# Kernel tuning notes

Measured on AMD Instinct MI355X. Metric: run time of the kernel, lower is better.

Reference implementation:

```python
import jax, jax.numpy as jnp
import numpy as np

D = 1024      # hidden_dim
H = 16        # num_heads
KV = 8        # num_kv_heads
HD = D // H   # head_size = 64
M = 3584      # intermediate_dim
E = 8         # num_local_experts
TOPK = 2      # num_experts_per_tok
EPS = 1e-6
ROPE_THETA = 10000.0


def setup_inputs() -> dict:
    key = jax.random.key(0)
    ks = jax.random.split(key, 12)
    s = 0.02
    B, S = 2, 1024
    return {
        "x": jax.random.normal(ks[0], (B, S, D), jnp.float32),
        "ln1_w": jnp.ones((D,), jnp.float32),
        "ln2_w": jnp.ones((D,), jnp.float32),
        "wq": jax.random.normal(ks[1], (D, H * HD), jnp.float32) * s,
        "wk": jax.random.normal(ks[2], (D, KV * HD), jnp.float32) * s,
        "wv": jax.random.normal(ks[3], (D, KV * HD), jnp.float32) * s,
        "wo": jax.random.normal(ks[4], (H * HD, D), jnp.float32) * s,
        "router_w": jax.random.normal(ks[5], (D, E), jnp.float32) * s,
        "w_gate": jax.random.normal(ks[6], (E, D, M), jnp.float32) * s,
        "w_up": jax.random.normal(ks[7], (E, D, M), jnp.float32) * s,
        "w_down": jax.random.normal(ks[8], (E, M, D), jnp.float32) * s,
    }


def _rmsnorm(x, w, eps=EPS):
    xf = x.astype(jnp.float32)
    var = jnp.mean(xf * xf, axis=-1, keepdims=True)
    return (xf * jax.lax.rsqrt(var + eps)).astype(x.dtype) * w


def _rope(q, k):
    # q: [B,S,H,HD], k: [B,S,KV,HD]
    S = q.shape[1]
    inv_freq = 1.0 / (ROPE_THETA ** (jnp.arange(0, HD, 2, dtype=jnp.float32) / HD))
    ang = jnp.arange(S, dtype=jnp.float32)[:, None] * inv_freq[None, :]  # [S, HD/2]
    cos = jnp.concatenate([jnp.cos(ang), jnp.cos(ang)], axis=-1)[None, :, None, :]
    sin = jnp.concatenate([jnp.sin(ang), jnp.sin(ang)], axis=-1)[None, :, None, :]

    def rot_half(t):
        t1, t2 = jnp.split(t, 2, axis=-1)
        return jnp.concatenate([-t2, t1], axis=-1)

    return q * cos + rot_half(q) * sin, k * cos + rot_half(k) * sin


def reference(x, ln1_w, ln2_w, wq, wk, wv, wo, router_w, w_gate, w_up, w_down):
    B, S, _ = x.shape

    # ---- self-attention block ----
    h = _rmsnorm(x, ln1_w)
    q = (h @ wq).reshape(B, S, H, HD)
    k = (h @ wk).reshape(B, S, KV, HD)
    v = (h @ wv).reshape(B, S, KV, HD)
    q, k = _rope(q, k)
    rep = H // KV
    k = jnp.repeat(k, rep, axis=2)  # [B,S,H,HD]
    v = jnp.repeat(v, rep, axis=2)
    scores = jnp.einsum("bqhd,bkhd->bhqk", q, k) / jnp.sqrt(jnp.float32(HD))
    causal = jnp.tril(jnp.ones((S, S), bool))
    scores = jnp.where(causal[None, None], scores, jnp.finfo(scores.dtype).min)
    attn = jax.nn.softmax(scores, axis=-1)
    ao = jnp.einsum("bhqk,bkhd->bqhd", attn, v).reshape(B, S, H * HD)
    x = x + ao @ wo

    # ---- sparse MoE block (top-2 routing, SwiGLU experts) ----
    h = _rmsnorm(x, ln2_w)
    logits = h @ router_w                       # [B,S,E]
    probs = jax.nn.softmax(logits, axis=-1)
    topv, topi = jax.lax.top_k(probs, TOPK)     # [B,S,K]
    topv = topv / jnp.sum(topv, axis=-1, keepdims=True)
    # dense combine weights [B,S,E]: zero for unselected experts
    weights = jnp.sum(jax.nn.one_hot(topi, E, dtype=h.dtype) * topv[..., None], axis=-2)
    gate = jnp.einsum("bsd,edm->bsem", h, w_gate)
    up = jnp.einsum("bsd,edm->bsem", h, w_up)
    act = jax.nn.silu(gate) * up * weights[..., None]
    moe = jnp.einsum("bsem,emd->bsd", act, w_down)
    return x + moe
```

## Files before the change

kernel.cpp:

```cpp
#include <hip/hip_runtime.h>

typedef __attribute__((ext_vector_type(8))) short short8;
typedef __attribute__((ext_vector_type(4))) float f32x4;
typedef unsigned int u32;

#define DI static __device__ __forceinline__

DI unsigned short f2bf(float f) {
  unsigned u = __builtin_bit_cast(unsigned, f);
  u += 0x7fffu + ((u >> 16) & 1u);
  return (unsigned short)(u >> 16);
}
DI float bf2f(unsigned short b) {
  unsigned u = ((unsigned)b) << 16;
  return __builtin_bit_cast(float, u);
}

DI void gload16(const unsigned short* g, unsigned short* l) {
  __builtin_amdgcn_global_load_lds(
      (const __attribute__((address_space(1))) u32*)g,
      (__attribute__((address_space(3))) u32*)l, 16, 0, 0);
}

static constexpr int NT   = 2048;
static constexpr int SEQ  = 1024;
static constexpr int DIM  = 1024;
static constexpr int NH   = 16;
static constexpr int NKV  = 8;
static constexpr int HD   = 64;
static constexpr int MDIM = 3584;
static constexpr int NE   = 8;
static constexpr int QW   = 2048;
static constexpr int GUW  = 2 * MDIM;

__global__ void __launch_bounds__(256) transpose_kernel(
    const float* __restrict__ in, unsigned short* __restrict__ out,
    int R, int C, size_t in_estride, size_t out_estride) {
  __shared__ unsigned short tl[64][66];
  int e = blockIdx.z;
  const float* ip = in + (size_t)e * in_estride;
  unsigned short* op = out + (size_t)e * out_estride;
  int c0 = blockIdx.x * 64, r0 = blockIdx.y * 64;
  int tid = threadIdx.x;
  {
    int lr = tid >> 4, lc = (tid & 15) * 4;
#pragma unroll
    for (int p = 0; p < 4; ++p) {
      int r = p * 16 + lr;
      float4 v = *(const float4*)(ip + (size_t)(r0 + r) * C + c0 + lc);
      tl[lc + 0][r] = f2bf(v.x);
      tl[lc + 1][r] = f2bf(v.y);
      tl[lc + 2][r] = f2bf(v.z);
      tl[lc + 3][r] = f2bf(v.w);
    }
  }
  __syncthreads();
  {
    int c = tid >> 2, rc = (tid & 3) * 16;
    unsigned short tmp[16];
#pragma unroll
    for (int j = 0; j < 8; ++j) {
      u32 w = *(const u32*)&tl[c][rc + j * 2];
      tmp[j * 2] = (unsigned short)w;
      tmp[j * 2 + 1] = (unsigned short)(w >> 16);
    }
    unsigned short* dst = op + (size_t)(c0 + c) * R + r0 + rc;
#pragma unroll
    for (int j = 0; j < 2; ++j)
      *(uint4*)(dst + j * 8) = *(const uint4*)&tmp[j * 8];
  }
}

__global__ void __launch_bounds__(256) rmsnorm_kernel(const float* __restrict__ x,
                                                      const float* __restrict__ w,
                                                      unsigned short* __restrict__ out) {
  int row = blockIdx.x;
  const float* xr = x + (size_t)row * DIM;
  int i = threadIdx.x * 4;
  float4 v = *(const float4*)(xr + i);
  float s = v.x * v.x + v.y * v.y + v.z * v.z + v.w * v.w;
  for (int o = 32; o; o >>= 1) s += __shfl_xor(s, o);
  __shared__ float red[4];
  if ((threadIdx.x & 63) == 0) red[threadIdx.x >> 6] = s;
  __syncthreads();
  s = red[0] + red[1] + red[2] + red[3];
  float r = rsqrtf(s * (1.0f / DIM) + 1e-6f);
  float4 wv = *(const float4*)(w + i);
  ushort4 o4;
  o4.x = f2bf(v.x * r * wv.x);
  o4.y = f2bf(v.y * r * wv.y);
  o4.z = f2bf(v.z * r * wv.z);
  o4.w = f2bf(v.w * r * wv.w);
  *(ushort4*)(out + (size_t)row * DIM + i) = o4;
}

template <int GATHER, int EPI>
__global__ void __launch_bounds__(256) gemmT_kernel(
    const unsigned short* __restrict__ A, int lda,
    const unsigned short* __restrict__ B, int ldb, size_t b_estride,
    void* __restrict__ Cv, int ldc,
    const float* __restrict__ resid,
    int M, int K,
    const int* __restrict__ lists, const int* __restrict__ cnt) {
  int e = blockIdx.z;
  int count = M;
  const int* lst = nullptr;
  if (GATHER != 0) {
    count = cnt[e];
    if (count <= 0) return;
    lst = lists + e * NT;
    B += b_estride * (size_t)e;
  }
  int m0 = blockIdx.y * 128;
  if (m0 >= count) return;
  int n0 = blockIdx.x * 128;

  __shared__ unsigned short sA[3][128 * 32];
  __shared__ unsigned short sB[3][128 * 32];

  int tid = threadIdx.x, w = tid >> 6, lane = tid & 63;
  int l15 = lane & 15, lhi = lane >> 4;

  int srow = w * 16 + (lane >> 2);
  int schunk = ((lane & 3) ^ ((lane >> 2) & 3)) * 8;
  const unsigned short *aSrc0, *aSrc1, *bSrc0, *bSrc1;
  {
    int mr0 = m0 + srow, mr1 = m0 + 64 + srow;
    int ar0, ar1;
    if (GATHER == 0) { ar0 = mr0; ar1 = mr1; }
    else {
      int c0i = mr0 < count ? mr0 : count - 1;
      int c1i = mr1 < count ? mr1 : count - 1;
      int p0 = lst[c0i], p1 = lst[c1i];
      ar0 = (GATHER == 1) ? (p0 >> 1) : p0;
      ar1 = (GATHER == 1) ? (p1 >> 1) : p1;
    }
    aSrc0 = A + (size_t)ar0 * lda + schunk;
    aSrc1 = A + (size_t)ar1 * lda + schunk;
    bSrc0 = B + (size_t)(n0 + srow) * ldb + schunk;
    bSrc1 = B + (size_t)(n0 + 64 + srow) * ldb + schunk;
  }
  unsigned ldst = (unsigned)(w * 16) * 32;

#define STAGE(buf, k0)                                   \
  do {                                                   \
    gload16(aSrc0 + (k0), &sA[buf][ldst]);               \
    gload16(aSrc1 + (k0), &sA[buf][ldst + 64 * 32]);     \
    gload16(bSrc0 + (k0), &sB[buf][ldst]);               \
    gload16(bSrc1 + (k0), &sB[buf][ldst + 64 * 32]);     \
  } while (0)

  f32x4 acc[4][4] = {};
  int wm = w >> 1, wn = w & 1;
  int aoff[4], boff[4];
#pragma unroll
  for (int t = 0; t < 4; ++t) {
    int row = wm * 64 + t * 16 + l15;
    aoff[t] = row * 32 + ((lhi ^ (row & 3)) * 8);
    int col = wn * 64 + t * 16 + l15;
    boff[t] = col * 32 + ((lhi ^ (col & 3)) * 8);
  }

  int nsteps = K / 32;
  STAGE(0, 0);
  if (nsteps > 1) STAGE(1, 32);

  int cur = 0, stg = 2;
  for (int t = 0; t < nsteps; ++t) {
    if (t + 1 < nsteps) asm volatile("s_waitcnt vmcnt(4)" ::: "memory");
    else                asm volatile("s_waitcnt vmcnt(0)" ::: "memory");
    __builtin_amdgcn_s_barrier();
    __builtin_amdgcn_sched_barrier(0);
    if (t + 2 < nsteps) STAGE(stg, (t + 2) * 32);
    const unsigned short* pa = sA[cur];
    const unsigned short* pb = sB[cur];
    short8 af[4], bfr[4];
#pragma unroll
    for (int q = 0; q < 4; ++q) {
      af[q] = *(const short8*)&pa[aoff[q]];
      bfr[q] = *(const short8*)&pb[boff[q]];
    }
    __builtin_amdgcn_s_setprio(1);
#pragma unroll
    for (int mi = 0; mi < 4; ++mi)
#pragma unroll
      for (int ni = 0; ni < 4; ++ni)
        acc[mi][ni] =
            __builtin_amdgcn_mfma_f32_16x16x32_bf16(af[mi], bfr[ni], acc[mi][ni], 0, 0, 0);
    __builtin_amdgcn_s_setprio(0);
    cur = (cur == 2) ? 0 : cur + 1;
    stg = (stg == 2) ? 0 : stg + 1;
  }
#undef STAGE

#pragma unroll
  for (int mi = 0; mi < 4; ++mi) {
#pragma unroll
    for (int r = 0; r < 4; ++r) {
      int mr = m0 + wm * 64 + mi * 16 + lhi * 4 + r;
      if (GATHER != 0 && mr >= count) continue;
      size_t crow = (GATHER != 0) ? (size_t)lst[mr] : (size_t)mr;
#pragma unroll
      for (int ni = 0; ni < 4; ++ni) {
        int n = n0 + wn * 64 + ni * 16 + l15;
        float val = acc[mi][ni][r];
        if (EPI == 0)
          ((unsigned short*)Cv)[crow * ldc + n] = f2bf(val);
        else if (EPI == 1)
          ((float*)Cv)[crow * ldc + n] = val + resid[crow * ldc + n];
        else
          ((float*)Cv)[crow * ldc + n] = val;
      }
    }
  }
}

__global__ void __launch_bounds__(256) rope_kernel(unsigned short* __restrict__ qkv) {
  int g = blockIdx.x * 256 + threadIdx.x;
  int i = g & 31;
  int hh = (g >> 5) % (NH + NKV);
  int tok = g / (32 * (NH + NKV));
  if (tok >= NT) return;
  int s = tok & (SEQ - 1);
  float inv = exp2f((float)i * (-13.287712379549449f / 32.0f));
  float ang = (float)s * inv;
  float sn = sinf(ang);
  float c = cosf(ang);
  int col = (hh < NH) ? hh * HD : DIM + (hh - NH) * HD;
  unsigned short* ptr = qkv + (size_t)tok * QW + col;
  float a = bf2f(ptr[i]), b2 = bf2f(ptr[i + 32]);
  ptr[i] = f2bf(a * c - b2 * sn);
  ptr[i + 32] = f2bf(b2 * c + a * sn);
}

__global__ void __launch_bounds__(64) attn_kernel(const unsigned short* __restrict__ qkv,
                                                  unsigned short* __restrict__ ao) {
  __shared__ unsigned short Ps[16 * 64];
  int bid = blockIdx.x;
  int qt = bid & 63;
  int h = (bid >> 6) & 15;
  int b = bid >> 10;
  int lane = threadIdx.x, l15 = lane & 15, lhi = lane >> 4;
  int q0 = qt * 16, kvh = h >> 1;
  int kcol = DIM + kvh * HD, vcol = DIM + NKV * HD + kvh * HD;

  const unsigned short* qp = qkv + ((size_t)(b * SEQ + q0 + l15)) * QW + h * HD + lhi * 8;
  short8 aq0 = *(const short8*)qp;
  short8 aq1 = *(const short8*)(qp + 32);

  float m[4] = {-1e30f, -1e30f, -1e30f, -1e30f};
  float l[4] = {0.f, 0.f, 0.f, 0.f};
  f32x4 accO[4] = {};

  int nkb = (qt >> 2) + 1;
  for (int kb_ = 0; kb_ < nkb; ++kb_) {
    int kbase = kb_ * 64;
    f32x4 s[4];
#pragma unroll
    for (int ct = 0; ct < 4; ++ct) {
      const unsigned short* kp =
          qkv + ((size_t)(b * SEQ + kbase + ct * 16 + l15)) * QW + kcol + lhi * 8;
      short8 k0v = *(const short8*)kp;
      short8 k1v = *(const short8*)(kp + 32);
      f32x4 a = {};
      a = __builtin_amdgcn_mfma_f32_16x16x32_bf16(aq0, k0v, a, 0, 0, 0);
      a = __builtin_amdgcn_mfma_f32_16x16x32_bf16(aq1, k1v, a, 0, 0, 0);
      int kpos = kbase + ct * 16 + l15;
#pragma unroll
      for (int r = 0; r < 4; ++r) {
        float v = a[r] * 0.125f;
        if (kpos > q0 + lhi * 4 + r) v = -1e30f;
        s[ct][r] = v;
      }
    }
    float nm[4], al[4], rs[4];
#pragma unroll
    for (int r = 0; r < 4; ++r) {
      float mb = fmaxf(fmaxf(s[0][r], s[1][r]), fmaxf(s[2][r], s[3][r]));
      mb = fmaxf(mb, __shfl_xor(mb, 1));
      mb = fmaxf(mb, __shfl_xor(mb, 2));
      mb = fmaxf(mb, __shfl_xor(mb, 4));
      mb = fmaxf(mb, __shfl_xor(mb, 8));
      nm[r] = fmaxf(m[r], mb);
      al[r] = __expf(m[r] - nm[r]);
      m[r] = nm[r];
      rs[r] = 0.f;
    }
#pragma unroll
    for (int ct = 0; ct < 4; ++ct) {
#pragma unroll
      for (int r = 0; r < 4; ++r) {
        float p = __expf(s[ct][r] - nm[r]);
        rs[r] += p;
        int q = lhi * 4 + r;
        Ps[q * 64 + ((ct * 16 + l15) ^ (lhi << 4))] = f2bf(p);
      }
    }
#pragma unroll
    for (int r = 0; r < 4; ++r) {
      rs[r] += __shfl_xor(rs[r], 1);
      rs[r] += __shfl_xor(rs[r], 2);
      rs[r] += __shfl_xor(rs[r], 4);
      rs[r] += __shfl_xor(rs[r], 8);
      l[r] = l[r] * al[r] + rs[r];
    }
#pragma unroll
    for (int dt = 0; dt < 4; ++dt)
#pragma unroll
      for (int r = 0; r < 4; ++r) accO[dt][r] *= al[r];

    int pswz = (l15 >> 2) << 4;
    short8 ap0 = *(const short8*)&Ps[l15 * 64 + ((lhi * 8) ^ pswz)];
    short8 ap1 = *(const short8*)&Ps[l15 * 64 + ((32 + lhi * 8) ^ pswz)];
#pragma unroll
    for (int dt = 0; dt < 4; ++dt) {
#pragma unroll
      for (int ks = 0; ks < 2; ++ks) {
        const unsigned short* vp =
            qkv + ((size_t)(b * SEQ + kbase + ks * 32 + lhi * 8)) * QW + vcol + dt * 16 + l15;
        short8 vf;
#pragma unroll
        for (int j = 0; j < 8; ++j) vf[j] = (short)vp[(size_t)j * QW];
        accO[dt] = __builtin_amdgcn_mfma_f32_16x16x32_bf16(ks ? ap1 : ap0, vf, accO[dt], 0, 0, 0);
      }
    }
  }
  float invl[4];
#pragma unroll
  for (int r = 0; r < 4; ++r) invl[r] = 1.f / l[r];
#pragma unroll
  for (int dt = 0; dt < 4; ++dt)
#pragma unroll
    for (int r = 0; r < 4; ++r)
      ao[((size_t)(b * SEQ + q0 + lhi * 4 + r)) * DIM + h * HD + dt * 16 + l15] =
          f2bf(accO[dt][r] * invl[r]);
}

__global__ void zero_cnt_kernel(int* __restrict__ cnt) {
  if (threadIdx.x < NE) cnt[threadIdx.x] = 0;
}

__global__ void __launch_bounds__(64) router_kernel(const float* __restrict__ x2,
                                                    const float* __restrict__ ln2w,
                                                    const float* __restrict__ rw,
                                                    float* __restrict__ wts,
                                                    int* __restrict__ cnt,
                                                    int* __restrict__ lists) {
  int t = blockIdx.x, lane = threadIdx.x;
  const float* xr = x2 + (size_t)t * DIM;
  float xs[16];
  double ssq = 0.0;
#pragma unroll
  for (int j = 0; j < 16; ++j) {
    xs[j] = xr[lane + j * 64];
    ssq += (double)xs[j] * xs[j];
  }
  for (int o = 32; o; o >>= 1) ssq += __shfl_xor(ssq, o);
  double r = rsqrt(ssq * (1.0 / DIM) + 1e-6);
  double p[NE] = {};
#pragma unroll
  for (int j = 0; j < 16; ++j) {
    int i = lane + j * 64;
    double hv = (double)xs[j] * r * (double)ln2w[i];
    const float* rwp = rw + (size_t)i * NE;
#pragma unroll
    for (int e = 0; e < NE; ++e) p[e] += hv * (double)rwp[e];
  }
  for (int o = 32; o; o >>= 1) {
#pragma unroll
    for (int e = 0; e < NE; ++e) p[e] += __shfl_xor(p[e], o);
  }
  if (lane == 0) {
    int i1 = 0;
    for (int e = 1; e < NE; ++e)
      if (p[e] > p[i1]) i1 = e;
    int i2 = (i1 == 0) ? 1 : 0;
    for (int e = 0; e < NE; ++e)
      if (e != i1 && p[e] > p[i2]) i2 = e;
    double mx = fmax(p[i1], p[i2]);
    double e1 = exp(p[i1] - mx), e2 = exp(p[i2] - mx);
    double inv = 1.0 / (e1 + e2);
    wts[t * 2] = (float)(e1 * inv);
    wts[t * 2 + 1] = (float)(e2 * inv);
    int pos1 = atomicAdd(&cnt[i1], 1);
    lists[i1 * NT + pos1] = t * 2;
    int pos2 = atomicAdd(&cnt[i2], 1);
    lists[i2 * NT + pos2] = t * 2 + 1;
  }
}

__global__ void __launch_bounds__(256) swiglu_kernel(const unsigned short* __restrict__ gu,
                                                     const float* __restrict__ wts,
                                                     unsigned short* __restrict__ act) {
  size_t i = ((size_t)blockIdx.x * 256 + threadIdx.x) * 8;
  int pid = (int)(i / MDIM);
  int mcol = (int)(i - (size_t)pid * MDIM);
  float w = wts[pid];
  const unsigned short* row = gu + (size_t)pid * GUW;
  short8 g8 = *(const short8*)(row + mcol);
  short8 u8 = *(const short8*)(row + MDIM + mcol);
  short8 o8;
#pragma unroll
  for (int j = 0; j < 8; ++j) {
    float gv = bf2f((unsigned short)g8[j]);
    float uv = bf2f((unsigned short)u8[j]);
    float sv = gv / (1.f + __expf(-gv));
    o8[j] = (short)f2bf(sv * uv * w);
  }
  *(short8*)(act + i) = o8;
}

__global__ void __launch_bounds__(256) combine_kernel(const float* __restrict__ x2,
                                                      const float* __restrict__ part,
                                                      float* __restrict__ out) {
  size_t idx = ((size_t)blockIdx.x * 256 + threadIdx.x) * 4;
  size_t t = idx >> 10;
  size_t d = idx & 1023;
  float4 a = *(const float4*)(x2 + idx);
  float4 b = *(const float4*)(part + (t * 2) * DIM + d);
  float4 c = *(const float4*)(part + (t * 2 + 1) * DIM + d);
  float4 o;
  o.x = a.x + b.x + c.x;
  o.y = a.y + b.y + c.y;
  o.z = a.z + b.z + c.z;
  o.w = a.w + b.w + c.w;
  *(float4*)(out + idx) = o;
}

extern "C" void kernel_launch(void* const* d_in, const int* in_sizes, int n_in,
                              void* d_out, int out_size, void* d_ws, size_t ws_size,
                              hipStream_t stream) {
  const float* x   = (const float*)d_in[0];
  const float* ln1 = (const float*)d_in[1];
  const float* ln2 = (const float*)d_in[2];
  const float* wq  = (const float*)d_in[3];
  const float* wk  = (const float*)d_in[4];
  const float* wv  = (const float*)d_in[5];
  const float* wo  = (const float*)d_in[6];
  const float* rw  = (const float*)d_in[7];
  const float* wg  = (const float*)d_in[8];
  const float* wu  = (const float*)d_in[9];
  const float* wd  = (const float*)d_in[10];
  float* out = (float*)d_out;

  char* p = (char*)d_ws;
  auto take = [&](size_t bytes) {
    char* q = p;
    p += (bytes + 255) & ~(size_t)255;
    return q;
  };
  unsigned short* wguT = (unsigned short*)take((size_t)NE * GUW * DIM * 2);
  unsigned short* wdT  = (unsigned short*)take((size_t)NE * DIM * MDIM * 2);
  float*          x2   = (float*)take((size_t)NT * DIM * 4);
  unsigned short* h2   = (unsigned short*)take((size_t)NT * DIM * 2);
  float*          part = (float*)take((size_t)2 * NT * DIM * 4);
  unsigned short* act  = (unsigned short*)take((size_t)2 * NT * MDIM * 2);
  float*          wtsb = (float*)take((size_t)2 * NT * 4);
  int*            cntb = (int*)take(NE * 4);
  int*            listsb = (int*)take((size_t)NE * NT * 4);
  char* X = p;
  unsigned short* wqkvT = (unsigned short*)X;
  unsigned short* woT   = wqkvT + (size_t)QW * DIM;
  unsigned short* h1    = woT + (size_t)DIM * DIM;
  unsigned short* qkv   = h1 + (size_t)NT * DIM;
  unsigned short* aob   = qkv + (size_t)NT * QW;
  unsigned short* gu    = (unsigned short*)X;

  transpose_kernel<<<dim3(16, 16, 1), 256, 0, stream>>>(wq, wqkvT, DIM, DIM, 0, 0);
  transpose_kernel<<<dim3(8, 16, 1), 256, 0, stream>>>(wk, wqkvT + (size_t)DIM * DIM, DIM, 512, 0, 0);
  transpose_kernel<<<dim3(8, 16, 1), 256, 0, stream>>>(wv, wqkvT + (size_t)(DIM + 512) * DIM, DIM, 512, 0, 0);
  transpose_kernel<<<dim3(16, 16, 1), 256, 0, stream>>>(wo, woT, DIM, DIM, 0, 0);
  transpose_kernel<<<dim3(56, 16, NE), 256, 0, stream>>>(
      wg, wguT, DIM, MDIM, (size_t)DIM * MDIM, (size_t)GUW * DIM);
  transpose_kernel<<<dim3(56, 16, NE), 256, 0, stream>>>(
      wu, wguT + (size_t)MDIM * DIM, DIM, MDIM, (size_t)DIM * MDIM, (size_t)GUW * DIM);
  transpose_kernel<<<dim3(16, 56, NE), 256, 0, stream>>>(
      wd, wdT, MDIM, DIM, (size_t)MDIM * DIM, (size_t)DIM * MDIM);

  rmsnorm_kernel<<<NT, 256, 0, stream>>>(x, ln1, h1);
  gemmT_kernel<0, 0><<<dim3(QW / 128, NT / 128, 1), 256, 0, stream>>>(
      h1, DIM, wqkvT, DIM, 0, qkv, QW, nullptr, NT, DIM, nullptr, nullptr);
  rope_kernel<<<(NT * (NH + NKV) * 32) / 256, 256, 0, stream>>>(qkv);
  attn_kernel<<<NT * NH / 16, 64, 0, stream>>>(qkv, aob);
  gemmT_kernel<0, 1><<<dim3(DIM / 128, NT / 128, 1), 256, 0, stream>>>(
      aob, DIM, woT, DIM, 0, x2, DIM, x, NT, DIM, nullptr, nullptr);

  rmsnorm_kernel<<<NT, 256, 0, stream>>>(x2, ln2, h2);
  zero_cnt_kernel<<<1, 64, 0, stream>>>(cntb);
  router_kernel<<<NT, 64, 0, stream>>>(x2, ln2, rw, wtsb, cntb, listsb);

  gemmT_kernel<1, 0><<<dim3(GUW / 128, 16, NE), 256, 0, stream>>>(
      h2, DIM, wguT, DIM, (size_t)GUW * DIM, gu, GUW, nullptr, 0, DIM, listsb, cntb);
  swiglu_kernel<<<(int)(((size_t)2 * NT * MDIM) / (256 * 8)), 256, 0, stream>>>(
      gu, wtsb, act);
  gemmT_kernel<2, 2><<<dim3(DIM / 128, 16, NE), 256, 0, stream>>>(
      act, MDIM, wdT, MDIM, (size_t)DIM * MDIM, part, DIM, nullptr, 0, MDIM, listsb, cntb);

  combine_kernel<<<(NT * DIM) / 1024, 256, 0, stream>>>(x2, part, out);
}
```

Before: 564.5 us.

## Widen gate/up GEMM tile to 256 columns and split-K the down projection

The GEMM kernel gets a compile-time N-tile width. The MoE gate/up projection now uses 128x256 tiles, which raises A-tile reuse and halves the number of gathered-row blocks, at the cost of more registers and LDS. The down projection is split along K into two halves across the z grid dimension, which doubles its block count for better CU occupancy. Each half writes to its own partial buffer and the combine kernel sums both halves, adding extra memory traffic and workspace.

```diff
diff --git a/kernel.cpp b/kernel.cpp
--- a/kernel.cpp
+++ b/kernel.cpp
@@ -94,15 +94,22 @@
   *(ushort4*)(out + (size_t)row * DIM + i) = o4;
 }
 
-template <int GATHER, int EPI>
+template <int GATHER, int EPI, int NNT>
 __global__ void __launch_bounds__(256) gemmT_kernel(
     const unsigned short* __restrict__ A, int lda,
     const unsigned short* __restrict__ B, int ldb, size_t b_estride,
     void* __restrict__ Cv, int ldc,
     const float* __restrict__ resid,
     int M, int K,
-    const int* __restrict__ lists, const int* __restrict__ cnt) {
-  int e = blockIdx.z;
+    const int* __restrict__ lists, const int* __restrict__ cnt,
+    int ks_count, size_t ks_stride) {
+  constexpr int BN = NNT * 32;
+  constexpr int NBLK = BN / 64;
+  int zz = blockIdx.z;
+  int e = zz / ks_count, ks = zz - e * ks_count;
+  int KL = K / ks_count;
+  int kbase = ks * KL;
+
   int count = M;
   const int* lst = nullptr;
   if (GATHER != 0) {
@@ -113,17 +120,18 @@
   }
   int m0 = blockIdx.y * 128;
   if (m0 >= count) return;
-  int n0 = blockIdx.x * 128;
+  int n0 = blockIdx.x * BN;
 
   __shared__ unsigned short sA[3][128 * 32];
-  __shared__ unsigned short sB[3][128 * 32];
+  __shared__ unsigned short sB[3][BN * 32];
 
   int tid = threadIdx.x, w = tid >> 6, lane = tid & 63;
   int l15 = lane & 15, lhi = lane >> 4;
 
   int srow = w * 16 + (lane >> 2);
   int schunk = ((lane & 3) ^ ((lane >> 2) & 3)) * 8;
-  const unsigned short *aSrc0, *aSrc1, *bSrc0, *bSrc1;
+  const unsigned short *aSrc0, *aSrc1;
+  const unsigned short* bSrc[NBLK];
   {
     int mr0 = m0 + srow, mr1 = m0 + 64 + srow;
     int ar0, ar1;
@@ -135,63 +143,69 @@
       ar0 = (GATHER == 1) ? (p0 >> 1) : p0;
       ar1 = (GATHER == 1) ? (p1 >> 1) : p1;
     }
-    aSrc0 = A + (size_t)ar0 * lda + schunk;
-    aSrc1 = A + (size_t)ar1 * lda + schunk;
-    bSrc0 = B + (size_t)(n0 + srow) * ldb + schunk;
-    bSrc1 = B + (size_t)(n0 + 64 + srow) * ldb + schunk;
+    aSrc0 = A + (size_t)ar0 * lda + kbase + schunk;
+    aSrc1 = A + (size_t)ar1 * lda + kbase + schunk;
+#pragma unroll
+    for (int s = 0; s < NBLK; ++s)
+      bSrc[s] = B + (size_t)(n0 + s * 64 + srow) * ldb + kbase + schunk;
   }
   unsigned ldst = (unsigned)(w * 16) * 32;
 
-#define STAGE(buf, k0)                                   \
-  do {                                                   \
-    gload16(aSrc0 + (k0), &sA[buf][ldst]);               \
-    gload16(aSrc1 + (k0), &sA[buf][ldst + 64 * 32]);     \
-    gload16(bSrc0 + (k0), &sB[buf][ldst]);               \
-    gload16(bSrc1 + (k0), &sB[buf][ldst + 64 * 32]);     \
-  } while (0)
-
-  f32x4 acc[4][4] = {};
+  auto stage = [&](int buf, int k0) {
+    gload16(aSrc0 + k0, &sA[buf][ldst]);
+    gload16(aSrc1 + k0, &sA[buf][ldst + 64 * 32]);
+#pragma unroll
+    for (int s = 0; s < NBLK; ++s)
+      gload16(bSrc[s] + k0, &sB[buf][ldst + s * 64 * 32]);
+  };
+
+  f32x4 acc[4][NNT] = {};
   int wm = w >> 1, wn = w & 1;
-  int aoff[4], boff[4];
+  int aoff[4], boff[NNT];
 #pragma unroll
   for (int t = 0; t < 4; ++t) {
     int row = wm * 64 + t * 16 + l15;
     aoff[t] = row * 32 + ((lhi ^ (row & 3)) * 8);
-    int col = wn * 64 + t * 16 + l15;
+  }
+#pragma unroll
+  for (int t = 0; t < NNT; ++t) {
+    int col = wn * (BN / 2) + t * 16 + l15;
     boff[t] = col * 32 + ((lhi ^ (col & 3)) * 8);
   }
 
-  int nsteps = K / 32;
-  STAGE(0, 0);
-  if (nsteps > 1) STAGE(1, 32);
+  int nsteps = KL / 32;
+  stage(0, 0);
+  if (nsteps > 1) stage(1, 32);
 
   int cur = 0, stg = 2;
   for (int t = 0; t < nsteps; ++t) {
-    if (t + 1 < nsteps) asm volatile("s_waitcnt vmcnt(4)" ::: "memory");
-    else                asm volatile("s_waitcnt vmcnt(0)" ::: "memory");
+    if (t + 1 < nsteps) {
+      if constexpr (NNT == 8) asm volatile("s_waitcnt vmcnt(6)" ::: "memory");
+      else                    asm volatile("s_waitcnt vmcnt(4)" ::: "memory");
+    } else {
+      asm volatile("s_waitcnt vmcnt(0)" ::: "memory");
+    }
     __builtin_amdgcn_s_barrier();
     __builtin_amdgcn_sched_barrier(0);
-    if (t + 2 < nsteps) STAGE(stg, (t + 2) * 32);
+    if (t + 2 < nsteps) stage(stg, (t + 2) * 32);
     const unsigned short* pa = sA[cur];
     const unsigned short* pb = sB[cur];
-    short8 af[4], bfr[4];
-#pragma unroll
-    for (int q = 0; q < 4; ++q) {
-      af[q] = *(const short8*)&pa[aoff[q]];
-      bfr[q] = *(const short8*)&pb[boff[q]];
-    }
+    short8 af[4], bfr[NNT];
+#pragma unroll
+    for (int q = 0; q < 4; ++q) af[q] = *(const short8*)&pa[aoff[q]];
+#pragma unroll
+    for (int q = 0; q < NNT; ++q) bfr[q] = *(const short8*)&pb[boff[q]];
     __builtin_amdgcn_s_setprio(1);
 #pragma unroll
     for (int mi = 0; mi < 4; ++mi)
 #pragma unroll
-      for (int ni = 0; ni < 4; ++ni)
+      for (int ni = 0; ni < NNT; ++ni)
         acc[mi][ni] =
             __builtin_amdgcn_mfma_f32_16x16x32_bf16(af[mi], bfr[ni], acc[mi][ni], 0, 0, 0);
     __builtin_amdgcn_s_setprio(0);
     cur = (cur == 2) ? 0 : cur + 1;
     stg = (stg == 2) ? 0 : stg + 1;
   }
-#undef STAGE
 
 #pragma unroll
   for (int mi = 0; mi < 4; ++mi) {
@@ -201,15 +215,15 @@
       if (GATHER != 0 && mr >= count) continue;
       size_t crow = (GATHER != 0) ? (size_t)lst[mr] : (size_t)mr;
 #pragma unroll
-      for (int ni = 0; ni < 4; ++ni) {
-        int n = n0 + wn * 64 + ni * 16 + l15;
+      for (int ni = 0; ni < NNT; ++ni) {
+        int n = n0 + wn * (BN / 2) + ni * 16 + l15;
         float val = acc[mi][ni][r];
         if (EPI == 0)
           ((unsigned short*)Cv)[crow * ldc + n] = f2bf(val);
         else if (EPI == 1)
           ((float*)Cv)[crow * ldc + n] = val + resid[crow * ldc + n];
         else
-          ((float*)Cv)[crow * ldc + n] = val;
+          ((float*)Cv)[(size_t)ks * ks_stride + crow * ldc + n] = val;
       }
     }
   }
@@ -413,17 +427,20 @@
 __global__ void __launch_bounds__(256) combine_kernel(const float* __restrict__ x2,
                                                       const float* __restrict__ part,
                                                       float* __restrict__ out) {
+  const size_t KSS = (size_t)2 * NT * DIM;
   size_t idx = ((size_t)blockIdx.x * 256 + threadIdx.x) * 4;
   size_t t = idx >> 10;
   size_t d = idx & 1023;
   float4 a = *(const float4*)(x2 + idx);
-  float4 b = *(const float4*)(part + (t * 2) * DIM + d);
-  float4 c = *(const float4*)(part + (t * 2 + 1) * DIM + d);
+  float4 b0 = *(const float4*)(part + (t * 2) * DIM + d);
+  float4 c0 = *(const float4*)(part + (t * 2 + 1) * DIM + d);
+  float4 b1 = *(const float4*)(part + KSS + (t * 2) * DIM + d);
+  float4 c1 = *(const float4*)(part + KSS + (t * 2 + 1) * DIM + d);
   float4 o;
-  o.x = a.x + b.x + c.x;
-  o.y = a.y + b.y + c.y;
-  o.z = a.z + b.z + c.z;
-  o.w = a.w + b.w + c.w;
+  o.x = a.x + b0.x + c0.x + b1.x + c1.x;
+  o.y = a.y + b0.y + c0.y + b1.y + c1.y;
+  o.z = a.z + b0.z + c0.z + b1.z + c1.z;
+  o.w = a.w + b0.w + c0.w + b1.w + c1.w;
   *(float4*)(out + idx) = o;
 }
 
@@ -453,7 +470,7 @@
   unsigned short* wdT  = (unsigned short*)take((size_t)NE * DIM * MDIM * 2);
   float*          x2   = (float*)take((size_t)NT * DIM * 4);
   unsigned short* h2   = (unsigned short*)take((size_t)NT * DIM * 2);
-  float*          part = (float*)take((size_t)2 * NT * DIM * 4);
+  float*          part = (float*)take((size_t)2 * 2 * NT * DIM * 4);
   unsigned short* act  = (unsigned short*)take((size_t)2 * NT * MDIM * 2);
   float*          wtsb = (float*)take((size_t)2 * NT * 4);
   int*            cntb = (int*)take(NE * 4);
@@ -478,23 +495,24 @@
       wd, wdT, MDIM, DIM, (size_t)MDIM * DIM, (size_t)DIM * MDIM);
 
   rmsnorm_kernel<<<NT, 256, 0, stream>>>(x, ln1, h1);
-  gemmT_kernel<0, 0><<<dim3(QW / 128, NT / 128, 1), 256, 0, stream>>>(
-      h1, DIM, wqkvT, DIM, 0, qkv, QW, nullptr, NT, DIM, nullptr, nullptr);
+  gemmT_kernel<0, 0, 4><<<dim3(QW / 128, NT / 128, 1), 256, 0, stream>>>(
+      h1, DIM, wqkvT, DIM, 0, qkv, QW, nullptr, NT, DIM, nullptr, nullptr, 1, 0);
   rope_kernel<<<(NT * (NH + NKV) * 32) / 256, 256, 0, stream>>>(qkv);
   attn_kernel<<<NT * NH / 16, 64, 0, stream>>>(qkv, aob);
-  gemmT_kernel<0, 1><<<dim3(DIM / 128, NT / 128, 1), 256, 0, stream>>>(
-      aob, DIM, woT, DIM, 0, x2, DIM, x, NT, DIM, nullptr, nullptr);
+  gemmT_kernel<0, 1, 4><<<dim3(DIM / 128, NT / 128, 1), 256, 0, stream>>>(
+      aob, DIM, woT, DIM, 0, x2, DIM, x, NT, DIM, nullptr, nullptr, 1, 0);
 
   rmsnorm_kernel<<<NT, 256, 0, stream>>>(x2, ln2, h2);
   zero_cnt_kernel<<<1, 64, 0, stream>>>(cntb);
   router_kernel<<<NT, 64, 0, stream>>>(x2, ln2, rw, wtsb, cntb, listsb);
 
-  gemmT_kernel<1, 0><<<dim3(GUW / 128, 16, NE), 256, 0, stream>>>(
-      h2, DIM, wguT, DIM, (size_t)GUW * DIM, gu, GUW, nullptr, 0, DIM, listsb, cntb);
+  gemmT_kernel<1, 0, 8><<<dim3(GUW / 256, 16, NE), 256, 0, stream>>>(
+      h2, DIM, wguT, DIM, (size_t)GUW * DIM, gu, GUW, nullptr, 0, DIM, listsb, cntb, 1, 0);
   swiglu_kernel<<<(int)(((size_t)2 * NT * MDIM) / (256 * 8)), 256, 0, stream>>>(
       gu, wtsb, act);
-  gemmT_kernel<2, 2><<<dim3(DIM / 128, 16, NE), 256, 0, stream>>>(
-      act, MDIM, wdT, MDIM, (size_t)DIM * MDIM, part, DIM, nullptr, 0, MDIM, listsb, cntb);
+  gemmT_kernel<2, 2, 4><<<dim3(DIM / 128, 16, NE * 2), 256, 0, stream>>>(
+      act, MDIM, wdT, MDIM, (size_t)DIM * MDIM, part, DIM, nullptr, 0, MDIM, listsb, cntb,
+      2, (size_t)2 * NT * DIM);
 
   combine_kernel<<<(NT * DIM) / 1024, 256, 0, stream>>>(x2, part, out);
 }
```

Measured after the change: 586.4 us. 3.9% more time.
